# Kernel tuning notes

Measured on AMD Instinct MI355X. Metric: run time of the kernel, lower is better.

## Reference

```python
import jax, jax.numpy as jnp
import numpy as np
jax.config.update("jax_enable_x64", True)

SR = 44100
STATE_SIZE = 4096
RG0, R10, C10, C20 = 1.0e6, 4.7e5, 3.3e-9, 1.0e-9

# Reconstructed DK-method incidence matrices (3 circuit nodes, 1 vsrc):
#   Vin at node1; C1 node1->node2; R1 node2->gnd; pot top node2->node3;
#   pot bottom node3->gnd; C2 node3->gnd; output at node3 (pot wiper).
_Nu = np.array([[1., 0., 0.]])
_Nx = np.array([[1., -1., 0.], [0., 0., 1.]])
_Nr = np.array([[0., 1., 0.]])
_Nv = np.array([[0., 1., -1.], [0., 0., 1.]])
_No = np.array([[0., 0., 1.]])


def _preamp_forward(x, cond, state, alpha_rg, alpha_r1, alpha_c1, alpha_c2, cond_w, cond_b):
    f64 = jnp.float64
    T = 1.0 / SR
    Nu, Nx, Nr, Nv, No = (jnp.asarray(m, f64) for m in (_Nu, _Nx, _Nr, _Nv, _No))
    Zm = jnp.eye(2, dtype=f64)
    n_nodes, n_vsrc = 3, 1
    zpad = jnp.zeros((2, n_vsrc), f64)
    Nvp = jnp.concatenate([Nv, zpad], axis=1)                      # [2,4]
    Nxp = jnp.concatenate([Nx, zpad], axis=1)                      # [2,4]
    Nop = jnp.concatenate([No, jnp.zeros((1, n_vsrc), f64)], 1)    # [1,4]
    Nup = jnp.concatenate([jnp.zeros((n_nodes, n_vsrc), f64), jnp.eye(n_vsrc, dtype=f64)], 0)  # [4,1]

    # component updates (sigmoid-trimmed around nominal values)
    RG = (0.9 + jax.nn.sigmoid(alpha_rg[0]).astype(f64) * 0.2) * RG0
    R1 = (0.99 + jax.nn.sigmoid(alpha_r1[0]).astype(f64) * 0.02) * R10
    C1 = (0.9 + jax.nn.sigmoid(alpha_c1[0]).astype(f64) * 0.2) * C10
    C2 = (0.9 + jax.nn.sigmoid(alpha_c2[0]).astype(f64) * 0.2) * C20
    Gr = jnp.reshape(1.0 / R1, (1, 1))
    Gx = jnp.diag(jnp.stack([2.0 * C1 / T, 2.0 * C2 / T]))

    # cond block: affine -> sigmoid -> log pot taper
    pot = jax.nn.sigmoid(cond[:, 0] * cond_w[0] + cond_b[0])
    p = jnp.clip((jnp.power(10.0, pot) - 1.0) / 9.0, 1e-4, 1.0 - 1e-4).astype(f64)  # [B]

    # state-space update
    top = jnp.concatenate([Nr.T @ Gr @ Nr + Nx.T @ Gx @ Nx, Nu.T], axis=1)
    bot = jnp.concatenate([Nu, jnp.zeros((n_vsrc, n_vsrc), f64)], axis=1)
    So_inv = jnp.linalg.inv(jnp.concatenate([top, bot], axis=0))   # [4,4]
    Q = Nvp @ So_inv @ Nvp.T                                        # [2,2]
    Ux = Nxp @ So_inv @ Nvp.T                                       # [2,2]
    Uo = Nop @ So_inv @ Nvp.T                                       # [1,2]
    Uu = Nup.T @ So_inv @ Nvp.T                                     # [1,2]
    ZGx = 2.0 * Zm @ Gx
    Ao = ZGx @ Nxp @ So_inv @ Nxp.T - Zm
    Bo = ZGx @ Nxp @ So_inv @ Nup
    Do = Nop @ So_inv @ Nxp.T
    Eo = Nop @ So_inv @ Nup

    d = jnp.stack([(1.0 - p) * RG, p * RG], axis=-1)                # [B,2]
    Rv = d[:, :, None] * jnp.eye(2, dtype=f64)                      # [B,2,2] diag
    RvQ = jnp.linalg.inv(Rv + Q)                                    # [B,2,2]

    ZGxUx = ZGx @ Ux
    A = Ao - ZGxUx @ RvQ @ Ux.T                                     # [B,2,2]
    Bm = Bo - ZGxUx @ RvQ @ Uu.T                                    # [B,2,1]
    Dm = Do - Uo @ RvQ @ Ux.T                                       # [B,1,2]
    Em = Eo - Uo @ RvQ @ Uu.T                                       # [B,1,1]

    # quadratic characteristic poly [1, -tr, det] (= real part of prod(z-eig))
    def poly2(M):
        tr = M[..., 0, 0] + M[..., 1, 1]
        det = M[..., 0, 0] * M[..., 1, 1] - M[..., 0, 1] * M[..., 1, 0]
        return jnp.stack([jnp.ones_like(tr), -tr, det], axis=-1)    # [B,3]

    den = poly2(A)
    num = poly2(A - Bm @ Dm) + (Em[:, 0] - 1.0) * den

    nb = 1 + STATE_SIZE // 2
    z = jnp.exp(-1j * jnp.linspace(0.0, jnp.pi, nb))                # complex128 [nb]

    def polyval(c):  # Horner, highest degree first
        c = c.astype(jnp.complex128)
        return (c[:, 0, None] * z + c[:, 1, None]) * z + c[:, 2, None]  # [B,nb]

    h = polyval(num) / polyval(den)                                 # [B,nb]

    L = x.shape[1]
    st = jnp.concatenate([state[:, L:, :], x], axis=1).astype(f64)  # [B,S,1]
    sf = jnp.fft.rfft(st, axis=1)                                   # [B,nb,1]
    out = jnp.fft.irfft(sf * h[:, :, None], axis=1).astype(jnp.float32)
    return out[:, -L:, :]


def setup_inputs() -> dict:
    key = jax.random.key(0)
    k0, k1, k2 = jax.random.split(key, 3)
    B, L = 2048, 2048
    return {
        "x": jax.random.normal(k0, (B, L, 1), dtype=jnp.float32),
        "cond": jax.random.uniform(k1, (B, 1), dtype=jnp.float32),
        "state": jax.random.normal(k2, (B, STATE_SIZE, 1), dtype=jnp.float32) * 0.1,
        "alpha_rg": jnp.zeros((1,), jnp.float32),
        "alpha_r1": jnp.zeros((1,), jnp.float32),
        "alpha_c1": jnp.zeros((1,), jnp.float32),
        "alpha_c2": jnp.zeros((1,), jnp.float32),
        "cond_w": jnp.ones((1,), jnp.float32),
        "cond_b": jnp.zeros((1,), jnp.float32),
    }


def reference(x, cond, state, alpha_rg, alpha_r1, alpha_c1, alpha_c2, cond_w, cond_b):
    return _preamp_forward(x, cond, state, alpha_rg, alpha_r1, alpha_c1, alpha_c2, cond_w, cond_b)
```

## Files before the change

kernel.cpp:

```cpp
#include <hip/hip_runtime.h>
#include <math.h>

#define NFFT 4096
#define HALF 2048
#define LSEG 2048
#define SSZ 4096

typedef float v2f __attribute__((ext_vector_type(2)));


static __device__ __forceinline__ v2f cmul(v2f a, v2f b) {
    return (v2f){ fmaf(-a.y, b.y, a.x * b.x), fmaf(a.y, b.x, a.x * b.y) };
}

static __device__ __forceinline__ int PAD(int i) { return i + (i >> 4); }

template <int SGN>
static __device__ __forceinline__ void dft16(v2f r[16]) {
    const float S = (float)SGN;
    v2f t[16];
#pragma unroll
    for (int n1 = 0; n1 < 4; ++n1) {
        v2f a = r[n1], b = r[n1 + 4], c = r[n1 + 8], d = r[n1 + 12];
        v2f A = a + c, B = b + d, C = a - c, D = b - d;
        v2f iD = (v2f){ -S * D.y, S * D.x };
        t[n1 * 4 + 0] = A + B;
        t[n1 * 4 + 1] = C + iD;
        t[n1 * 4 + 2] = A - B;
        t[n1 * 4 + 3] = C - iD;
    }
    const float CC[10] = {1.f, 0.92387953251f, 0.70710678119f, 0.38268343236f, 0.f,
                          -0.38268343236f, -0.70710678119f, -0.92387953251f, -1.f, -0.92387953251f};
    const float SS[10] = {0.f, 0.38268343236f, 0.70710678119f, 0.92387953251f, 1.f,
                          0.92387953251f, 0.70710678119f, 0.38268343236f, 0.f, -0.38268343236f};
#pragma unroll
    for (int n1 = 1; n1 < 4; ++n1) {
#pragma unroll
        for (int m2 = 1; m2 < 4; ++m2) {
            const int k = n1 * m2;
            t[n1 * 4 + m2] = cmul(t[n1 * 4 + m2], (v2f){CC[k], S * SS[k]});
        }
    }
#pragma unroll
    for (int m2 = 0; m2 < 4; ++m2) {
        v2f a = t[m2], b = t[4 + m2], c = t[8 + m2], d = t[12 + m2];
        v2f A = a + c, B = b + d, C = a - c, D = b - d;
        v2f iD = (v2f){ -S * D.y, S * D.x };
        r[m2]      = A + B;
        r[m2 + 4]  = C + iD;
        r[m2 + 8]  = A - B;
        r[m2 + 12] = C - iD;
    }
}

static __device__ __forceinline__ void twiddle_chain(v2f r[16], v2f w1) {
    v2f w2 = cmul(w1, w1);
    v2f w3 = cmul(w2, w1);
    v2f w4 = cmul(w2, w2);
    v2f w5 = cmul(w4, w1);
    v2f w6 = cmul(w4, w2);
    v2f w7 = cmul(w4, w3);
    v2f w8 = cmul(w4, w4);
    r[1] = cmul(r[1], w1);   r[2] = cmul(r[2], w2);
    r[3] = cmul(r[3], w3);   r[4] = cmul(r[4], w4);
    r[5] = cmul(r[5], w5);   r[6] = cmul(r[6], w6);
    r[7] = cmul(r[7], w7);   r[8] = cmul(r[8], w8);
    r[9]  = cmul(r[9],  cmul(w8, w1));
    r[10] = cmul(r[10], cmul(w8, w2));
    r[11] = cmul(r[11], cmul(w8, w3));
    r[12] = cmul(r[12], cmul(w8, w4));
    r[13] = cmul(r[13], cmul(w8, w5));
    r[14] = cmul(r[14], cmul(w8, w6));
    r[15] = cmul(r[15], cmul(w8, w7));
}

__global__ __launch_bounds__(256)
void preamp_fft_kernel(const float* __restrict__ x,
                       const float* __restrict__ state,
                       const float* __restrict__ cond,
                       const float* __restrict__ a_rg,
                       const float* __restrict__ a_r1,
                       const float* __restrict__ a_c1,
                       const float* __restrict__ a_c2,
                       const float* __restrict__ cond_w,
                       const float* __restrict__ cond_b,
                       float* __restrict__ out, int B) {
    __shared__ v2f a_s[NFFT + NFFT / 16];
    __shared__ float cf[10];

    const int t = threadIdx.x;
    const int b0 = 2 * blockIdx.x;
    const int b1 = (b0 + 1 < B) ? b0 + 1 : b0;

    const float* st0 = state + (size_t)b0 * SSZ + (SSZ - LSEG);
    const float* xb0 = x + (size_t)b0 * LSEG;
    const float* st1 = state + (size_t)b1 * SSZ + (SSZ - LSEG);
    const float* xb1 = x + (size_t)b1 * LSEG;

    for (int i = t; i < NFFT; i += 256) {
        float fa, fb;
        if (i < LSEG) { fa = st0[i]; fb = st1[i]; }
        else          { fa = xb0[i - LSEG]; fb = xb1[i - LSEG]; }
        a_s[PAD(i)] = (v2f){fa, fb};
    }

    if ((t & 127) == 0) {
        const int who = t >> 7;
        const int bb = who ? b1 : b0;

        const double RG = (0.9 + (double)(1.0f / (1.0f + expf(-a_rg[0]))) * 0.2) * 1.0e6;
        const double R1 = (0.99 + (double)(1.0f / (1.0f + expf(-a_r1[0]))) * 0.02) * 4.7e5;
        const double C1 = (0.9 + (double)(1.0f / (1.0f + expf(-a_c1[0]))) * 0.2) * 3.3e-9;
        const double C2 = (0.9 + (double)(1.0f / (1.0f + expf(-a_c2[0]))) * 0.2) * 1.0e-9;
        const double g1 = 1.0 / R1;
        const double gc1 = 2.0 * C1 * 44100.0;
        const double gc2 = 2.0 * C2 * 44100.0;

        float zf = cond[bb] * cond_w[0] + cond_b[0];
        float pot = 1.0f / (1.0f + expf(-zf));
        float prf = (powf(10.0f, pot) - 1.0f) / 9.0f;
        prf = fminf(fmaxf(prf, 1e-4f), 1.0f - 1e-4f);
        const double p = (double)prf;

        const double ds = gc1 + g1;
        double S[4][4] = {
            {0.0, 0.0,        0.0,       1.0},
            {0.0, 1.0 / ds,   0.0,       gc1 / ds},
            {0.0, 0.0,        1.0 / gc2, 0.0},
            {1.0, gc1 / ds,   0.0,       -gc1 * g1 / ds}};

        double Q00 = S[1][1] - S[1][2] - S[2][1] + S[2][2];
        double Q01 = S[1][2] - S[2][2];
        double Q10 = S[2][1] - S[2][2];
        double Q11 = S[2][2];

        double Ux00 = S[0][1] - S[0][2] - S[1][1] + S[1][2];
        double Ux01 = S[0][2] - S[1][2];
        double Ux10 = S[2][1] - S[2][2];
        double Ux11 = S[2][2];

        double Uo0 = S[2][1] - S[2][2], Uo1 = S[2][2];
        double Uu0 = S[3][1] - S[3][2], Uu1 = S[3][2];

        double P00 = S[0][0] - S[0][1] - S[1][0] + S[1][1];
        double P01 = S[0][2] - S[1][2];
        double P10 = S[2][0] - S[2][1];
        double P11 = S[2][2];

        double Ao00 = 2.0 * gc1 * P00 - 1.0, Ao01 = 2.0 * gc1 * P01;
        double Ao10 = 2.0 * gc2 * P10,       Ao11 = 2.0 * gc2 * P11 - 1.0;

        double Bo0 = 2.0 * gc1 * (S[0][3] - S[1][3]);
        double Bo1 = 2.0 * gc2 * S[2][3];

        double Do0 = S[2][0] - S[2][1], Do1 = S[2][2];
        double Eo  = S[2][3];

        double T00 = 2.0 * gc1 * Ux00, T01 = 2.0 * gc1 * Ux01;
        double T10 = 2.0 * gc2 * Ux10, T11 = 2.0 * gc2 * Ux11;

        double d0 = (1.0 - p) * RG, d1v = p * RG;
        double M00 = d0 + Q00, M01 = Q01, M10 = Q10, M11 = d1v + Q11;
        double idet = 1.0 / (M00 * M11 - M01 * M10);
        double G00 =  M11 * idet, G01 = -M01 * idet;
        double G10 = -M10 * idet, G11 =  M00 * idet;

        double TG00 = T00 * G00 + T01 * G10, TG01 = T00 * G01 + T01 * G11;
        double TG10 = T10 * G00 + T11 * G10, TG11 = T10 * G01 + T11 * G11;

        double A00 = Ao00 - (TG00 * Ux00 + TG01 * Ux01);
        double A01 = Ao01 - (TG00 * Ux10 + TG01 * Ux11);
        double A10 = Ao10 - (TG10 * Ux00 + TG11 * Ux01);
        double A11 = Ao11 - (TG10 * Ux10 + TG11 * Ux11);

        double Bm0 = Bo0 - (TG00 * Uu0 + TG01 * Uu1);
        double Bm1 = Bo1 - (TG10 * Uu0 + TG11 * Uu1);

        double w0v = Uo0 * G00 + Uo1 * G10, w1v = Uo0 * G01 + Uo1 * G11;
        double Dm0 = Do0 - (w0v * Ux00 + w1v * Ux01);
        double Dm1 = Do1 - (w0v * Ux10 + w1v * Ux11);
        double Em  = Eo  - (w0v * Uu0 + w1v * Uu1);

        double den1 = -(A00 + A11);
        double den2 = A00 * A11 - A01 * A10;
        double Mm00 = A00 - Bm0 * Dm0, Mm01 = A01 - Bm0 * Dm1;
        double Mm10 = A10 - Bm1 * Dm0, Mm11 = A11 - Bm1 * Dm1;
        double num0 = Em;
        double num1 = -(Mm00 + Mm11) + (Em - 1.0) * den1;
        double num2 = (Mm00 * Mm11 - Mm01 * Mm10) + (Em - 1.0) * den2;

        cf[who * 5 + 0] = (float)num0;
        cf[who * 5 + 1] = (float)num1;
        cf[who * 5 + 2] = (float)(num0 + num1 + num2);
        cf[who * 5 + 3] = (float)den1;
        cf[who * 5 + 4] = (float)(1.0 + den1 + den2);
    }
    __syncthreads();

    const float TW4096 = 0.00153398078788564f;
    const float TW256  = 0.02454369260617026f;
    const float HW4096 = 0.00076699039394282f;

    v2f r[16];

#pragma unroll
    for (int m = 0; m < 16; ++m) r[m] = a_s[PAD(t + 256 * m)];
    dft16<-1>(r);
    {
        float sw, cw;
        __sincosf((float)t * TW4096, &sw, &cw);
        twiddle_chain(r, (v2f){cw, -sw});
    }
#pragma unroll
    for (int m = 0; m < 16; ++m) a_s[PAD(t + 256 * m)] = r[m];
    __syncthreads();

    {
        const int sub = t >> 4, j = t & 15;
        const int base = sub * 256 + j;
#pragma unroll
        for (int m = 0; m < 16; ++m) r[m] = a_s[PAD(base + 16 * m)];
        dft16<-1>(r);
        float sw, cw;
        __sincosf((float)j * TW256, &sw, &cw);
        twiddle_chain(r, (v2f){cw, -sw});
#pragma unroll
        for (int m = 0; m < 16; ++m) a_s[PAD(base + 16 * m)] = r[m];
    }
    __syncthreads();

    {
        const int base = 16 * t;
#pragma unroll
        for (int m = 0; m < 16; ++m) r[m] = a_s[PAD(base + m)];
        dft16<-1>(r);
        const int klo = ((t & 15) << 4) | (t >> 4);
        __syncthreads();
#pragma unroll
        for (int m = 0; m < 16; ++m) a_s[PAD((m << 8) | klo)] = r[m];
    }
    __syncthreads();

    {
        const float an0 = cf[0], an1 = cf[1], asn = cf[2], ad1 = cf[3], asd = cf[4];
        const float bn0 = cf[5], bn1 = cf[6], bsn = cf[7], bd1 = cf[8], bsd = cf[9];

        for (int i = t; i <= HALF; i += 256) {
            const int k  = i;
            const int kr = (NFFT - i) & (NFFT - 1);
            v2f Wk = a_s[PAD(k)];
            v2f Wr = a_s[PAD(kr)];
            float Xar = 0.5f * (Wk.x + Wr.x), Xai = 0.5f * (Wk.y - Wr.y);
            float Xbr = 0.5f * (Wk.y + Wr.y), Xbi = 0.5f * (Wr.x - Wk.x);
            float sh, ch;
            __sincosf((float)k * HW4096, &sh, &ch);
            float m2s = -2.0f * sh;
            float ur = m2s * sh, ui = m2s * ch;
            float pr = ur + 2.0f;
            float tar = an0 * pr + an1, tai = an0 * ui;
            float nr = asn + ur * tar - ui * tai, ni = ur * tai + ui * tar;
            float tbr = pr + ad1;
            float dr = asd + ur * tbr - ui * ui, di = ur * ui + ui * tbr;
            float inv = __builtin_amdgcn_rcpf(dr * dr + di * di);
            float Har = (nr * dr + ni * di) * inv, Hai = (ni * dr - nr * di) * inv;
            tar = bn0 * pr + bn1; tai = bn0 * ui;
            nr = bsn + ur * tar - ui * tai; ni = ur * tai + ui * tar;
            tbr = pr + bd1;
            dr = bsd + ur * tbr - ui * ui; di = ur * ui + ui * tbr;
            inv = __builtin_amdgcn_rcpf(dr * dr + di * di);
            float Hbr = (nr * dr + ni * di) * inv, Hbi = (ni * dr - nr * di) * inv;

            float Yar = Har * Xar - Hai * Xai, Yai = Har * Xai + Hai * Xar;
            float Ybr = Hbr * Xbr - Hbi * Xbi, Ybi = Hbr * Xbi + Hbi * Xbr;
            a_s[PAD(k)] = (v2f){Yar - Ybi, Yai + Ybr};
            if (kr != k) a_s[PAD(kr)] = (v2f){Yar + Ybi, Ybr - Yai};
        }
    }
    __syncthreads();

    {
        const int base = 16 * t;
        const int klo = ((t & 15) << 4) | (t >> 4);
#pragma unroll
        for (int m = 0; m < 16; ++m) r[m] = a_s[PAD((m << 8) | klo)];
        dft16<1>(r);
        __syncthreads();
#pragma unroll
        for (int m = 0; m < 16; ++m) a_s[PAD(base + m)] = r[m];
    }
    __syncthreads();

    {
        const int sub = t >> 4, j = t & 15;
        const int base = sub * 256 + j;
#pragma unroll
        for (int m = 0; m < 16; ++m) r[m] = a_s[PAD(base + 16 * m)];
        float sw, cw;
        __sincosf((float)j * TW256, &sw, &cw);
        twiddle_chain(r, (v2f){cw, sw});
        dft16<1>(r);
#pragma unroll
        for (int m = 0; m < 16; ++m) a_s[PAD(base + 16 * m)] = r[m];
    }
    __syncthreads();

    {
#pragma unroll
        for (int m = 0; m < 16; ++m) r[m] = a_s[PAD(t + 256 * m)];
        float sw, cw;
        __sincosf((float)t * TW4096, &sw, &cw);
        twiddle_chain(r, (v2f){cw, sw});
        dft16<1>(r);
        const float scale = 1.0f / (float)NFFT;
        float* ob0 = out + (size_t)b0 * LSEG;
        float* ob1 = out + (size_t)b1 * LSEG;
#pragma unroll
        for (int m = 8; m < 16; ++m) {
            const int idx = t + 256 * (m - 8);
            float ya = r[m].x * scale;
            float yb = (b1 != b0) ? r[m].y * scale : ya;
            ob0[idx] = ya;
            ob1[idx] = yb;
        }
    }
}

extern "C" void kernel_launch(void* const* d_in, const int* in_sizes, int n_in,
                              void* d_out, int out_size, void* d_ws, size_t ws_size,
                              hipStream_t stream) {
    const float* x     = (const float*)d_in[0];
    const float* cond  = (const float*)d_in[1];
    const float* state = (const float*)d_in[2];
    const float* a_rg  = (const float*)d_in[3];
    const float* a_r1  = (const float*)d_in[4];
    const float* a_c1  = (const float*)d_in[5];
    const float* a_c2  = (const float*)d_in[6];
    const float* c_w   = (const float*)d_in[7];
    const float* c_b   = (const float*)d_in[8];
    float* out = (float*)d_out;

    const int B = in_sizes[1];

    preamp_fft_kernel<<<dim3((B + 1) / 2), dim3(256), 0, stream>>>(
        x, state, cond, a_rg, a_r1, a_c1, a_c2, c_w, c_b, out, B);
}
```

Baseline: 121.2 us.

## Replace FFT circular convolution with partial-fraction IIR parallel scan

```diff
diff --git a/kernel.cpp b/kernel.cpp
--- a/kernel.cpp
+++ b/kernel.cpp
@@ -2,80 +2,13 @@
 #include <math.h>
 
 #define NFFT 4096
-#define HALF 2048
 #define LSEG 2048
 #define SSZ 4096
 
-typedef float v2f __attribute__((ext_vector_type(2)));
-
-
-static __device__ __forceinline__ v2f cmul(v2f a, v2f b) {
-    return (v2f){ fmaf(-a.y, b.y, a.x * b.x), fmaf(a.y, b.x, a.x * b.y) };
-}
-
-static __device__ __forceinline__ int PAD(int i) { return i + (i >> 4); }
-
-template <int SGN>
-static __device__ __forceinline__ void dft16(v2f r[16]) {
-    const float S = (float)SGN;
-    v2f t[16];
-#pragma unroll
-    for (int n1 = 0; n1 < 4; ++n1) {
-        v2f a = r[n1], b = r[n1 + 4], c = r[n1 + 8], d = r[n1 + 12];
-        v2f A = a + c, B = b + d, C = a - c, D = b - d;
-        v2f iD = (v2f){ -S * D.y, S * D.x };
-        t[n1 * 4 + 0] = A + B;
-        t[n1 * 4 + 1] = C + iD;
-        t[n1 * 4 + 2] = A - B;
-        t[n1 * 4 + 3] = C - iD;
-    }
-    const float CC[10] = {1.f, 0.92387953251f, 0.70710678119f, 0.38268343236f, 0.f,
-                          -0.38268343236f, -0.70710678119f, -0.92387953251f, -1.f, -0.92387953251f};
-    const float SS[10] = {0.f, 0.38268343236f, 0.70710678119f, 0.92387953251f, 1.f,
-                          0.92387953251f, 0.70710678119f, 0.38268343236f, 0.f, -0.38268343236f};
-#pragma unroll
-    for (int n1 = 1; n1 < 4; ++n1) {
-#pragma unroll
-        for (int m2 = 1; m2 < 4; ++m2) {
-            const int k = n1 * m2;
-            t[n1 * 4 + m2] = cmul(t[n1 * 4 + m2], (v2f){CC[k], S * SS[k]});
-        }
-    }
-#pragma unroll
-    for (int m2 = 0; m2 < 4; ++m2) {
-        v2f a = t[m2], b = t[4 + m2], c = t[8 + m2], d = t[12 + m2];
-        v2f A = a + c, B = b + d, C = a - c, D = b - d;
-        v2f iD = (v2f){ -S * D.y, S * D.x };
-        r[m2]      = A + B;
-        r[m2 + 4]  = C + iD;
-        r[m2 + 8]  = A - B;
-        r[m2 + 12] = C - iD;
-    }
-}
-
-static __device__ __forceinline__ void twiddle_chain(v2f r[16], v2f w1) {
-    v2f w2 = cmul(w1, w1);
-    v2f w3 = cmul(w2, w1);
-    v2f w4 = cmul(w2, w2);
-    v2f w5 = cmul(w4, w1);
-    v2f w6 = cmul(w4, w2);
-    v2f w7 = cmul(w4, w3);
-    v2f w8 = cmul(w4, w4);
-    r[1] = cmul(r[1], w1);   r[2] = cmul(r[2], w2);
-    r[3] = cmul(r[3], w3);   r[4] = cmul(r[4], w4);
-    r[5] = cmul(r[5], w5);   r[6] = cmul(r[6], w6);
-    r[7] = cmul(r[7], w7);   r[8] = cmul(r[8], w8);
-    r[9]  = cmul(r[9],  cmul(w8, w1));
-    r[10] = cmul(r[10], cmul(w8, w2));
-    r[11] = cmul(r[11], cmul(w8, w3));
-    r[12] = cmul(r[12], cmul(w8, w4));
-    r[13] = cmul(r[13], cmul(w8, w5));
-    r[14] = cmul(r[14], cmul(w8, w6));
-    r[15] = cmul(r[15], cmul(w8, w7));
-}
-
-__global__ __launch_bounds__(256)
-void preamp_fft_kernel(const float* __restrict__ x,
+typedef float v4f __attribute__((ext_vector_type(4)));
+
+__global__ __launch_bounds__(256, 4)
+void preamp_iir_kernel(const float* __restrict__ x,
                        const float* __restrict__ state,
                        const float* __restrict__ cond,
                        const float* __restrict__ a_rg,
@@ -85,29 +18,38 @@
                        const float* __restrict__ cond_w,
                        const float* __restrict__ cond_b,
                        float* __restrict__ out, int B) {
-    __shared__ v2f a_s[NFFT + NFFT / 16];
-    __shared__ float cf[10];
+    __shared__ float cf[13];
+    __shared__ float Tw[2][4];
+    __shared__ float Tot[2];
 
     const int t = threadIdx.x;
-    const int b0 = 2 * blockIdx.x;
-    const int b1 = (b0 + 1 < B) ? b0 + 1 : b0;
-
-    const float* st0 = state + (size_t)b0 * SSZ + (SSZ - LSEG);
-    const float* xb0 = x + (size_t)b0 * LSEG;
-    const float* st1 = state + (size_t)b1 * SSZ + (SSZ - LSEG);
-    const float* xb1 = x + (size_t)b1 * LSEG;
-
-    for (int i = t; i < NFFT; i += 256) {
-        float fa, fb;
-        if (i < LSEG) { fa = st0[i]; fb = st1[i]; }
-        else          { fa = xb0[i - LSEG]; fb = xb1[i - LSEG]; }
-        a_s[PAD(i)] = (v2f){fa, fb};
-    }
-
-    if ((t & 127) == 0) {
-        const int who = t >> 7;
-        const int bb = who ? b1 : b0;
-
+    const int b = blockIdx.x;
+    const int lane = t & 63;
+    const int wv = t >> 6;
+
+    const float* xb  = x + (size_t)b * LSEG;
+    const float* stb = state + (size_t)b * SSZ + (SSZ - LSEG);
+
+    float s[16];
+    if (t < 128) {
+#pragma unroll
+        for (int u = 0; u < 4; ++u) {
+            const int g0 = 4092 - 16 * t - 4 * u;
+            v4f v = *(const v4f*)(xb + (g0 - LSEG));
+            s[4 * u + 0] = v.w; s[4 * u + 1] = v.z;
+            s[4 * u + 2] = v.y; s[4 * u + 3] = v.x;
+        }
+    } else {
+#pragma unroll
+        for (int u = 0; u < 4; ++u) {
+            const int g0 = 4092 - 16 * t - 4 * u;
+            v4f v = *(const v4f*)(stb + g0);
+            s[4 * u + 0] = v.w; s[4 * u + 1] = v.z;
+            s[4 * u + 2] = v.y; s[4 * u + 3] = v.x;
+        }
+    }
+
+    if (t == 0) {
         const double RG = (0.9 + (double)(1.0f / (1.0f + expf(-a_rg[0]))) * 0.2) * 1.0e6;
         const double R1 = (0.99 + (double)(1.0f / (1.0f + expf(-a_r1[0]))) * 0.02) * 4.7e5;
         const double C1 = (0.9 + (double)(1.0f / (1.0f + expf(-a_c1[0]))) * 0.2) * 3.3e-9;
@@ -116,7 +58,7 @@
         const double gc1 = 2.0 * C1 * 44100.0;
         const double gc2 = 2.0 * C2 * 44100.0;
 
-        float zf = cond[bb] * cond_w[0] + cond_b[0];
+        float zf = cond[b] * cond_w[0] + cond_b[0];
         float pot = 1.0f / (1.0f + expf(-zf));
         float prf = (powf(10.0f, pot) - 1.0f) / 9.0f;
         prf = fminf(fmaxf(prf, 1e-4f), 1.0f - 1e-4f);
@@ -189,138 +131,106 @@
         double num1 = -(Mm00 + Mm11) + (Em - 1.0) * den1;
         double num2 = (Mm00 * Mm11 - Mm01 * Mm10) + (Em - 1.0) * den2;
 
-        cf[who * 5 + 0] = (float)num0;
-        cf[who * 5 + 1] = (float)num1;
-        cf[who * 5 + 2] = (float)(num0 + num1 + num2);
-        cf[who * 5 + 3] = (float)den1;
-        cf[who * 5 + 4] = (float)(1.0 + den1 + den2);
+        double trA  = A00 + A11;
+        double disc = den1 * den1 - 4.0 * den2;
+        double sq   = sqrt(disc > 0.0 ? disc : 0.0);
+        double L1d  = 0.5 * (trA + sq);
+        double L2d  = 0.5 * (trA - sq);
+        double nv1 = (num0 * L1d + num1) * L1d + num2;
+        double nv2 = (num0 * L2d + num1) * L2d + num2;
+        double C0d =  num2 / den2;
+        double C1d =  nv1 / (L1d * sq);
+        double C2d = -nv2 / (L2d * sq);
+        double a2 = L1d * L1d, a4 = a2 * a2, a8 = a4 * a4, F16a = a8 * a8;
+        double a32 = F16a * F16a, a64 = a32 * a32, a128 = a64 * a64,
+               a256 = a128 * a128, a512 = a256 * a256, F1ka = a512 * a512;
+        double F4ka = (F1ka * F1ka) * (F1ka * F1ka);
+        double b2 = L2d * L2d, b4 = b2 * b2, b8 = b4 * b4, F16b = b8 * b8;
+        double b32 = F16b * F16b, b64 = b32 * b32, b128 = b64 * b64,
+               b256 = b128 * b128, b512 = b256 * b256, F1kb = b512 * b512;
+        double F4kb = (F1kb * F1kb) * (F1kb * F1kb);
+
+        cf[0]  = (float)L1d;
+        cf[1]  = (float)L2d;
+        cf[2]  = (float)C0d;
+        cf[3]  = (float)C1d;
+        cf[4]  = (float)C2d;
+        cf[5]  = (float)F16a;
+        cf[6]  = (float)F16b;
+        cf[7]  = (float)(16.0 * log2(L1d));
+        cf[8]  = (float)(16.0 * log2(L2d));
+        cf[9]  = (float)F1ka;
+        cf[10] = (float)F1kb;
+        cf[11] = (float)(1.0 / (1.0 - F4ka));
+        cf[12] = (float)(1.0 / (1.0 - F4kb));
     }
     __syncthreads();
 
-    const float TW4096 = 0.00153398078788564f;
-    const float TW256  = 0.02454369260617026f;
-    const float HW4096 = 0.00076699039394282f;
-
-    v2f r[16];
-
-#pragma unroll
-    for (int m = 0; m < 16; ++m) r[m] = a_s[PAD(t + 256 * m)];
-    dft16<-1>(r);
-    {
-        float sw, cw;
-        __sincosf((float)t * TW4096, &sw, &cw);
-        twiddle_chain(r, (v2f){cw, -sw});
-    }
-#pragma unroll
-    for (int m = 0; m < 16; ++m) a_s[PAD(t + 256 * m)] = r[m];
+    const float lam1 = cf[0], lam2 = cf[1];
+    const float c0 = cf[2], c1 = cf[3], c2 = cf[4];
+    const float f16a = cf[5], f16b = cf[6];
+    const float l2a = cf[7], l2b = cf[8];
+    const float f1ka = cf[9], f1kb = cf[10];
+    const float ioma = cf[11], iomb = cf[12];
+
+    float w1 = 0.0f, w2 = 0.0f;
+#pragma unroll
+    for (int j = 0; j < 16; ++j) {
+        w1 = fmaf(lam1, w1, s[j]);
+        w2 = fmaf(lam2, w2, s[j]);
+    }
+
+    float f1 = f16a, f2 = f16b;
+#pragma unroll
+    for (int d = 1; d < 64; d <<= 1) {
+        float o1 = __shfl_up(w1, d);
+        float o2 = __shfl_up(w2, d);
+        if (lane >= d) { w1 = fmaf(f1, o1, w1); w2 = fmaf(f2, o2, w2); }
+        f1 *= f1; f2 *= f2;
+    }
+    if (lane == 63) { Tw[0][wv] = w1; Tw[1][wv] = w2; }
     __syncthreads();
 
-    {
-        const int sub = t >> 4, j = t & 15;
-        const int base = sub * 256 + j;
-#pragma unroll
-        for (int m = 0; m < 16; ++m) r[m] = a_s[PAD(base + 16 * m)];
-        dft16<-1>(r);
-        float sw, cw;
-        __sincosf((float)j * TW256, &sw, &cw);
-        twiddle_chain(r, (v2f){cw, -sw});
-#pragma unroll
-        for (int m = 0; m < 16; ++m) a_s[PAD(base + 16 * m)] = r[m];
-    }
+    float S1 = 0.0f, S2 = 0.0f;
+#pragma unroll
+    for (int v = 0; v < 3; ++v) {
+        if (v < wv) {
+            S1 = fmaf(S1, f1ka, Tw[0][v]);
+            S2 = fmaf(S2, f1kb, Tw[1][v]);
+        }
+    }
+    const float el1 = exp2f((float)lane * l2a);
+    const float el2 = exp2f((float)lane * l2b);
+    w1 = fmaf(el1 * f16a, S1, w1);
+    w2 = fmaf(el2 * f16b, S2, w2);
+    if (t == 255) { Tot[0] = w1; Tot[1] = w2; }
+    float p1 = __shfl_up(w1, 1); if (lane == 0) p1 = S1;
+    float p2 = __shfl_up(w2, 1); if (lane == 0) p2 = S2;
     __syncthreads();
 
-    {
-        const int base = 16 * t;
-#pragma unroll
-        for (int m = 0; m < 16; ++m) r[m] = a_s[PAD(base + m)];
-        dft16<-1>(r);
-        const int klo = ((t & 15) << 4) | (t >> 4);
-        __syncthreads();
-#pragma unroll
-        for (int m = 0; m < 16; ++m) a_s[PAD((m << 8) | klo)] = r[m];
-    }
-    __syncthreads();
-
-    {
-        const float an0 = cf[0], an1 = cf[1], asn = cf[2], ad1 = cf[3], asd = cf[4];
-        const float bn0 = cf[5], bn1 = cf[6], bsn = cf[7], bd1 = cf[8], bsd = cf[9];
-
-        for (int i = t; i <= HALF; i += 256) {
-            const int k  = i;
-            const int kr = (NFFT - i) & (NFFT - 1);
-            v2f Wk = a_s[PAD(k)];
-            v2f Wr = a_s[PAD(kr)];
-            float Xar = 0.5f * (Wk.x + Wr.x), Xai = 0.5f * (Wk.y - Wr.y);
-            float Xbr = 0.5f * (Wk.y + Wr.y), Xbi = 0.5f * (Wr.x - Wk.x);
-            float sh, ch;
-            __sincosf((float)k * HW4096, &sh, &ch);
-            float m2s = -2.0f * sh;
-            float ur = m2s * sh, ui = m2s * ch;
-            float pr = ur + 2.0f;
-            float tar = an0 * pr + an1, tai = an0 * ui;
-            float nr = asn + ur * tar - ui * tai, ni = ur * tai + ui * tar;
-            float tbr = pr + ad1;
-            float dr = asd + ur * tbr - ui * ui, di = ur * ui + ui * tbr;
-            float inv = __builtin_amdgcn_rcpf(dr * dr + di * di);
-            float Har = (nr * dr + ni * di) * inv, Hai = (ni * dr - nr * di) * inv;
-            tar = bn0 * pr + bn1; tai = bn0 * ui;
-            nr = bsn + ur * tar - ui * tai; ni = ur * tai + ui * tar;
-            tbr = pr + bd1;
-            dr = bsd + ur * tbr - ui * ui; di = ur * ui + ui * tbr;
-            inv = __builtin_amdgcn_rcpf(dr * dr + di * di);
-            float Hbr = (nr * dr + ni * di) * inv, Hbi = (ni * dr - nr * di) * inv;
-
-            float Yar = Har * Xar - Hai * Xai, Yai = Har * Xai + Hai * Xar;
-            float Ybr = Hbr * Xbr - Hbi * Xbi, Ybi = Hbr * Xbi + Hbi * Xbr;
-            a_s[PAD(k)] = (v2f){Yar - Ybi, Yai + Ybr};
-            if (kr != k) a_s[PAD(kr)] = (v2f){Yar + Ybi, Ybr - Yai};
-        }
-    }
-    __syncthreads();
-
-    {
-        const int base = 16 * t;
-        const int klo = ((t & 15) << 4) | (t >> 4);
-#pragma unroll
-        for (int m = 0; m < 16; ++m) r[m] = a_s[PAD((m << 8) | klo)];
-        dft16<1>(r);
-        __syncthreads();
-#pragma unroll
-        for (int m = 0; m < 16; ++m) a_s[PAD(base + m)] = r[m];
-    }
-    __syncthreads();
-
-    {
-        const int sub = t >> 4, j = t & 15;
-        const int base = sub * 256 + j;
-#pragma unroll
-        for (int m = 0; m < 16; ++m) r[m] = a_s[PAD(base + 16 * m)];
-        float sw, cw;
-        __sincosf((float)j * TW256, &sw, &cw);
-        twiddle_chain(r, (v2f){cw, sw});
-        dft16<1>(r);
-#pragma unroll
-        for (int m = 0; m < 16; ++m) a_s[PAD(base + 16 * m)] = r[m];
-    }
-    __syncthreads();
-
-    {
-#pragma unroll
-        for (int m = 0; m < 16; ++m) r[m] = a_s[PAD(t + 256 * m)];
-        float sw, cw;
-        __sincosf((float)t * TW4096, &sw, &cw);
-        twiddle_chain(r, (v2f){cw, sw});
-        dft16<1>(r);
-        const float scale = 1.0f / (float)NFFT;
-        float* ob0 = out + (size_t)b0 * LSEG;
-        float* ob1 = out + (size_t)b1 * LSEG;
-#pragma unroll
-        for (int m = 8; m < 16; ++m) {
-            const int idx = t + 256 * (m - 8);
-            float ya = r[m].x * scale;
-            float yb = (b1 != b0) ? r[m].y * scale : ya;
-            ob0[idx] = ya;
-            ob1[idx] = yb;
+    if (t < 128) {
+        const float K1 = Tot[0] * ioma;
+        const float K2 = Tot[1] * iomb;
+        float base1 = el1 * (wv ? f1ka : 1.0f) * lam1 * K1;
+        float base2 = el2 * (wv ? f1kb : 1.0f) * lam2 * K2;
+        float w1r = p1, w2r = p2;
+        float yv[16];
+#pragma unroll
+        for (int j = 0; j < 16; ++j) {
+            w1r = fmaf(lam1, w1r, s[j]);
+            w2r = fmaf(lam2, w2r, s[j]);
+            float acc = c1 * (w1r + base1);
+            acc = fmaf(c2, (w2r + base2), acc);
+            yv[j] = fmaf(c0, s[j], acc);
+            base1 *= lam1; base2 *= lam2;
+        }
+        float* ob = out + (size_t)b * LSEG;
+#pragma unroll
+        for (int u = 0; u < 4; ++u) {
+            v4f o;
+            o.x = yv[4 * u + 3]; o.y = yv[4 * u + 2];
+            o.z = yv[4 * u + 1]; o.w = yv[4 * u + 0];
+            *(v4f*)(ob + (2044 - 16 * t - 4 * u)) = o;
         }
     }
 }
@@ -341,6 +251,6 @@
 
     const int B = in_sizes[1];
 
-    preamp_fft_kernel<<<dim3((B + 1) / 2), dim3(256), 0, stream>>>(
+    preamp_iir_kernel<<<dim3(B), dim3(256), 0, stream>>>(
         x, state, cond, a_rg, a_r1, a_c1, a_c2, c_w, c_b, out, B);
 }
```

Result: faster. 106.1 us (-12.4%).
